# Performance work log

Measured on AMD Instinct MI355X. Metric: run time of the kernel, lower is better.

## Reference

```python
import jax, jax.numpy as jnp
import numpy as np

B, S, D = 1, 2048, 4096          # batch, seqlen, model dim
H, KVH, HD = 32, 8, 128          # query heads, kv heads, head dim
W = 1024                         # sliding window
ROPE_THETA = 10000.0


def _rope(t, cos, sin):
    # t: [b, s, h, hd]; complex pairing matches torch.view_as_complex on reshape(..., hd//2, 2)
    a = t[..., 0::2]
    b = t[..., 1::2]
    out_r = a * cos - b * sin
    out_i = a * sin + b * cos
    return jnp.stack([out_r, out_i], axis=-1).reshape(t.shape)


def setup_inputs() -> dict:
    key = jax.random.key(0)
    ks = jax.random.split(key, 5)
    x = jax.random.normal(ks[0], (1, B, S, D), dtype=jnp.float32)
    wq = jax.random.normal(ks[1], (H * HD, D), dtype=jnp.float32) * 0.02
    wk = jax.random.normal(ks[2], (KVH * HD, D), dtype=jnp.float32) * 0.02
    wv = jax.random.normal(ks[3], (KVH * HD, D), dtype=jnp.float32) * 0.02
    wo = jax.random.normal(ks[4], (D, H * HD), dtype=jnp.float32) * 0.02
    # rotary frequencies: freqs_cis[s, hd/2] = exp(i * s * theta^{-2k/hd})
    inv_freq = 1.0 / (ROPE_THETA ** (jnp.arange(0, HD, 2, dtype=jnp.float32) / HD))
    angles = jnp.arange(S, dtype=jnp.float32)[:, None] * inv_freq[None, :]  # [S, HD/2]
    freqs_cos = jnp.cos(angles)
    freqs_sin = jnp.sin(angles)
    # sliding-window causal mask (additive)
    i = jnp.arange(S)
    allowed = (i[:, None] >= i[None, :]) & (i[:, None] - i[None, :] < W)
    mask = jnp.where(allowed, 0.0, -1e9).astype(jnp.float32)
    positions = jnp.arange(S, dtype=jnp.int64)
    return {"x": x, "wq": wq, "wk": wk, "wv": wv, "wo": wo,
            "freqs_cos": freqs_cos, "freqs_sin": freqs_sin,
            "mask": mask, "positions": positions}


def reference(x, wq, wk, wv, wo, freqs_cos, freqs_sin, mask, positions):
    xs = x[0]                                   # [B, S, D]
    xq = (xs @ wq.T).reshape(B, S, H, HD)
    xk = (xs @ wk.T).reshape(B, S, KVH, HD)
    xv = (xs @ wv.T).reshape(B, S, KVH, HD)
    cos = freqs_cos[None, :, None, :]           # [1, S, 1, HD/2]
    sin = freqs_sin[None, :, None, :]
    xq = _rope(xq, cos, sin)
    xk = _rope(xk, cos, sin)
    # GQA: repeat_interleave kv heads to match query heads (prefill path)
    rep = H // KVH
    k = jnp.repeat(xk, rep, axis=2)             # [B, S, H, HD]
    v = jnp.repeat(xv, rep, axis=2)
    scale = HD ** -0.5
    scores = jnp.einsum('bqhd,bkhd->bhqk', xq, k) * scale + mask[None, None]
    probs = jax.nn.softmax(scores, axis=-1)
    out = jnp.einsum('bhqk,bkhd->bqhd', probs, v).reshape(B, S, H * HD)
    return (out @ wo.T)[None]                   # [1, B, S, D]
```

## Files before the change

### kernel.cpp

```cpp
#include <hip/hip_runtime.h>
#include <hip/hip_bf16.h>


typedef __attribute__((ext_vector_type(8))) short short8;
typedef __attribute__((ext_vector_type(4))) float floatx4;
typedef unsigned short u16;
typedef unsigned int u32;

__device__ __forceinline__ u16 f2bf(float f) {
  u32 u = __builtin_bit_cast(u32, f);
  u32 r = u + 0x7FFFu + ((u >> 16) & 1u);
  return (u16)(r >> 16);
}

#define GLDS16(g, l)                                                     \
  __builtin_amdgcn_global_load_lds(                                      \
      (const __attribute__((address_space(1))) u32*)(g),                 \
      (__attribute__((address_space(3))) u32*)(l), 16, 0, 0)

__global__ __launch_bounds__(256) void cast_all(
    const float* __restrict__ x, const float* __restrict__ wq,
    const float* __restrict__ wk, const float* __restrict__ wv,
    const float* __restrict__ wo, u16* __restrict__ xb, u16* __restrict__ wqb,
    u16* __restrict__ wkb, u16* __restrict__ wvb, u16* __restrict__ wob) {
  const int tid = blockIdx.x * blockDim.x + threadIdx.x;
  const int stride = gridDim.x * blockDim.x;
  auto seg = [&](const float* __restrict__ in, u16* __restrict__ out, int n4) {
    for (int i = tid; i < n4; i += stride) {
      float4 v = ((const float4*)in)[i];
      ushort4 o;
      o.x = f2bf(v.x); o.y = f2bf(v.y); o.z = f2bf(v.z); o.w = f2bf(v.w);
      ((ushort4*)out)[i] = o;
    }
  };
  seg(x, xb, 2097152);
  seg(wq, wqb, 4194304);
  seg(wk, wkb, 1048576);
  seg(wv, wvb, 1048576);
  seg(wo, wob, 4194304);
}

template <int IS_QKV>
__global__ __launch_bounds__(512, 2) void gemm_t(
    const u16* __restrict__ A, const u16* __restrict__ B, void* __restrict__ Cq,
    u16* __restrict__ Ck, u16* __restrict__ Cv, const float* __restrict__ fcos,
    const float* __restrict__ fsin) {
  constexpr int BM = IS_QKV ? 256 : 128;
  constexpr int BN = IS_QKV ? 192 : 256;
  constexpr int MFR = BM / 32;
  constexpr int AH = MFR / 2;
  constexpr int NFR = BN / 64;
  constexpr int WC = BN / 4;
  constexpr int ABYTES = BM * 64;
  constexpr int BUFSZ = ABYTES + BN * 64;
  __shared__ u16 lds[3 * BUFSZ / 2];
  const int K = 4096;

  int bm, bx;
  if constexpr (IS_QKV) {
    bm = blockIdx.x & 7;
    bx = blockIdx.x >> 3;
  } else {
    const int xcd = blockIdx.x & 7;
    const int j = blockIdx.x >> 3;
    bm = xcd * 2 + (j & 1);
    bx = j >> 1;
  }
  const int m0 = bm * BM, n0 = bx * BN;

  const int t = threadIdx.x, l = t & 63, w = t >> 6;
  const int li = l & 15, g = l >> 4;
  const int wm = w >> 2, wn = w & 3;

  const int rr = t >> 2;
  const int ssw = (t & 3) ^ ((rr >> 1) & 3);
  const u16* gA = A + (size_t)(m0 + rr) * K + ssw * 8;
  const u16* gB = B + (size_t)(n0 + rr) * K + ssw * 8;
  const int dA = t * 16;

  auto stageA = [&](int p, int kt) {
    char* base = (char*)lds + p * BUFSZ;
    GLDS16(gA + kt, base + dA);
    if constexpr (IS_QKV)
      GLDS16(gA + (size_t)128 * K + kt, base + 8192 + dA);
  };
  auto stageB = [&](int p, int kt) {
    char* base = (char*)lds + p * BUFSZ + ABYTES;
    GLDS16(gB + kt, base + dA);
    if constexpr (IS_QKV) {
      if (t < 256)
        GLDS16(gB + (size_t)128 * K + kt, base + 8192 + dA);
    } else {
      GLDS16(gB + (size_t)128 * K + kt, base + 8192 + dA);
    }
  };
  auto waitL = [&]() {
    if constexpr (IS_QKV) {
      if (t < 256) asm volatile("s_waitcnt vmcnt(4)" ::: "memory");
      else         asm volatile("s_waitcnt vmcnt(3)" ::: "memory");
    } else {
      asm volatile("s_waitcnt vmcnt(3)" ::: "memory");
    }
  };

  int offA[MFR], offB[NFR];
#pragma unroll
  for (int mf = 0; mf < MFR; mf++) {
    int r = wm * (BM / 2) + mf * 16 + li;
    offA[mf] = r * 64 + ((g ^ ((r >> 1) & 3)) << 4);
  }
#pragma unroll
  for (int nf = 0; nf < NFR; nf++) {
    int r = wn * WC + nf * 16 + li;
    offB[nf] = ABYTES + r * 64 + ((g ^ ((r >> 1) & 3)) << 4);
  }

  floatx4 acc[MFR][NFR] = {};
  const int NT = K / 32;

  stageA(0, 0); stageB(0, 0);
  stageA(1, 32); stageB(1, 32);
  waitL();
  __builtin_amdgcn_s_barrier();

  int p = 0;
  for (int tt = 0; tt < NT; ++tt) {
    int p2 = p + 2; if (p2 >= 3) p2 -= 3;
    const char* ab = (const char*)lds + p * BUFSZ;
    const int kt2 = (tt + 2) * 32;
    const bool pre = (tt + 2 < NT);
    short8 afr[AH], bfr[NFR];
#pragma unroll
    for (int nf = 0; nf < NFR; nf++) bfr[nf] = *(const short8*)(ab + offB[nf]);
#pragma unroll
    for (int mf = 0; mf < AH; mf++) afr[mf] = *(const short8*)(ab + offA[mf]);
    if (pre) stageA(p2, kt2);
    __builtin_amdgcn_sched_barrier(0);
    __builtin_amdgcn_s_barrier();
    asm volatile("s_waitcnt lgkmcnt(0)" ::: "memory");
    __builtin_amdgcn_sched_barrier(0);
    __builtin_amdgcn_s_setprio(1);
#pragma unroll
    for (int mf = 0; mf < AH; mf++)
#pragma unroll
      for (int nf = 0; nf < NFR; nf++)
        acc[mf][nf] = __builtin_amdgcn_mfma_f32_16x16x32_bf16(afr[mf], bfr[nf], acc[mf][nf], 0, 0, 0);
    __builtin_amdgcn_s_setprio(0);
    __builtin_amdgcn_sched_barrier(0);
    __builtin_amdgcn_s_barrier();
#pragma unroll
    for (int mf = 0; mf < AH; mf++) afr[mf] = *(const short8*)(ab + offA[AH + mf]);
    if (pre) stageB(p2, kt2);
    __builtin_amdgcn_sched_barrier(0);
    __builtin_amdgcn_s_barrier();
    asm volatile("s_waitcnt lgkmcnt(0)" ::: "memory");
    __builtin_amdgcn_sched_barrier(0);
    __builtin_amdgcn_s_setprio(1);
#pragma unroll
    for (int mf = 0; mf < AH; mf++)
#pragma unroll
      for (int nf = 0; nf < NFR; nf++)
        acc[AH + mf][nf] = __builtin_amdgcn_mfma_f32_16x16x32_bf16(afr[mf], bfr[nf], acc[AH + mf][nf], 0, 0, 0);
    __builtin_amdgcn_s_setprio(0);
    if (pre) {
      waitL();
    } else if (tt + 1 < NT) {
      asm volatile("s_waitcnt vmcnt(0)" ::: "memory");
    }
    __builtin_amdgcn_sched_barrier(0);
    __builtin_amdgcn_s_barrier();
    p = p + 1; if (p >= 3) p -= 3;
  }

  const float scale = 0.08838834764831845f;
#pragma unroll
  for (int mf = 0; mf < MFR; mf++) {
#pragma unroll
    for (int nf = 0; nf < NFR; nf++) {
      const int row0 = m0 + wm * (BM / 2) + mf * 16 + 4 * g;
      const int c = n0 + wn * WC + nf * 16 + li;
      if constexpr (!IS_QKV) {
        float* Cf = (float*)Cq;
#pragma unroll
        for (int r = 0; r < 4; r++) Cf[(size_t)(row0 + r) * 4096 + c] = acc[mf][nf][r];
      } else {
        if (c < 5120) {
          const int hd = c & 127;
          const int pp = hd >> 1;
          const bool even = (hd & 1) == 0;
#pragma unroll
          for (int r = 0; r < 4; r++) {
            const int row = row0 + r;
            float cv = fcos[row * 64 + pp];
            float sv = fsin[row * 64 + pp];
            float v = acc[mf][nf][r];
            float pv = __shfl_xor(v, 1);
            float o = even ? (v * cv - pv * sv) : (pv * sv + v * cv);
            if (c < 4096) {
              ((u16*)Cq)[(size_t)row * 4096 + c] = f2bf(o * scale);
            } else {
              Ck[(size_t)row * 1024 + (c - 4096)] = f2bf(o);
            }
          }
        } else {
          u32 lo = (u32)f2bf(acc[mf][nf][0]) | ((u32)f2bf(acc[mf][nf][1]) << 16);
          u32 hi = (u32)f2bf(acc[mf][nf][2]) | ((u32)f2bf(acc[mf][nf][3]) << 16);
          uint2 val; val.x = lo; val.y = hi;
          *(uint2*)(&Cv[(size_t)(c - 5120) * 2048 + row0]) = val;
        }
      }
    }
  }
}

__global__ __launch_bounds__(256) void attn_kernel(const u16* __restrict__ Q,
                                                   const u16* __restrict__ K,
                                                   const u16* __restrict__ Vt,
                                                   u16* __restrict__ O) {
  __shared__ u16 Ks[2][64 * 128];
  __shared__ u16 Vs[2][128 * 64];
  __shared__ u16 Ps[4][16 * 72];

  const int t = threadIdx.x, l = t & 63, w = t >> 6;
  const int li = l & 15, g = l >> 4;
  const int q0 = blockIdx.x * 64;
  const int h = blockIdx.y;
  const int kvh = h >> 2;
  const int qw = q0 + w * 16;

  short8 qf[4];
  {
    const u16* qp = Q + (size_t)(qw + li) * 4096 + h * 128 + g * 8;
#pragma unroll
    for (int kk = 0; kk < 4; kk++) qf[kk] = *(const short8*)(qp + kk * 32);
  }

  const u16* gK[4];
  const u16* gV[4];
  int ldsOff[4];
#pragma unroll
  for (int i = 0; i < 4; i++) {
    int rK = 16 * w + 4 * i + (l >> 4);
    int sK = (l & 15) ^ (rK & 7);
    gK[i] = K + (size_t)rK * 1024 + kvh * 128 + sK * 8;
    int rV = 32 * w + 8 * i + (l >> 3);
    int sV = (l & 7) ^ (rV & 7);
    gV[i] = Vt + (size_t)(kvh * 128 + rV) * 2048 + sV * 8;
    ldsOff[i] = (4 * w + i) * 1024;
  }

  int offK[4][4];
#pragma unroll
  for (int n = 0; n < 4; n++) {
    int r = 16 * n + li;
#pragma unroll
    for (int kk = 0; kk < 4; kk++)
      offK[n][kk] = r * 256 + (((kk * 4 + g) ^ (r & 7)) << 4);
  }
  int offV[2][8];
#pragma unroll
  for (int kb = 0; kb < 2; kb++)
#pragma unroll
    for (int dt = 0; dt < 8; dt++) {
      int d = dt * 16 + li;
      offV[kb][dt] = d * 128 + (((kb * 4 + g) ^ (d & 7)) << 4);
    }

  float mrow[4] = {-1e30f, -1e30f, -1e30f, -1e30f};
  float lsum[4] = {0.f, 0.f, 0.f, 0.f};
  floatx4 accO[8] = {};

  int klo = q0 - 1023;
  if (klo < 0) klo = 0;
  klo &= ~63;
  const int nt = (q0 + 64 - klo) >> 6;

  auto stage = [&](int buf, int k0) {
    char* ksb = (char*)&Ks[buf][0];
    char* vsb = (char*)&Vs[buf][0];
#pragma unroll
    for (int i = 0; i < 4; i++) GLDS16(gK[i] + (size_t)k0 * 1024, ksb + ldsOff[i]);
#pragma unroll
    for (int i = 0; i < 4; i++) GLDS16(gV[i] + k0, vsb + ldsOff[i]);
  };

  stage(0, klo);
  asm volatile("s_waitcnt vmcnt(0)" ::: "memory");
  __builtin_amdgcn_s_barrier();

  for (int it = 0; it < nt; it++) {
    const int k0 = klo + (it << 6);
    if (it + 1 < nt) stage((it + 1) & 1, k0 + 64);

    if (k0 <= qw + 15 && k0 + 63 >= qw - 1023) {
      const char* kb = (const char*)&Ks[it & 1][0];
      const char* vb = (const char*)&Vs[it & 1][0];
      floatx4 s[4] = {};
      __builtin_amdgcn_s_setprio(1);
#pragma unroll
      for (int kk = 0; kk < 4; kk++)
#pragma unroll
        for (int n = 0; n < 4; n++) {
          short8 kf = *(const short8*)(kb + offK[n][kk]);
          s[n] = __builtin_amdgcn_mfma_f32_16x16x32_bf16(qf[kk], kf, s[n], 0, 0, 0);
        }
      __builtin_amdgcn_s_setprio(0);
      const bool full = (k0 + 63 <= qw) && (k0 >= qw + 15 - 1023);
      if (!full) {
#pragma unroll
        for (int n = 0; n < 4; n++) {
          const int kc = k0 + n * 16 + li;
#pragma unroll
          for (int r = 0; r < 4; r++) {
            const int qr = qw + 4 * g + r;
            if (kc > qr || qr - kc > 1023) s[n][r] = -__builtin_inff();
          }
        }
      }
      float rm[4];
#pragma unroll
      for (int r = 0; r < 4; r++)
        rm[r] = fmaxf(fmaxf(s[0][r], s[1][r]), fmaxf(s[2][r], s[3][r]));
#pragma unroll
      for (int msk = 1; msk <= 8; msk <<= 1)
#pragma unroll
        for (int r = 0; r < 4; r++) rm[r] = fmaxf(rm[r], __shfl_xor(rm[r], msk));
      float al[4];
#pragma unroll
      for (int r = 0; r < 4; r++) {
        float mn = fmaxf(mrow[r], rm[r]);
        al[r] = __expf(mrow[r] - mn);
        mrow[r] = mn;
        lsum[r] *= al[r];
      }
#pragma unroll
      for (int dt = 0; dt < 8; dt++)
#pragma unroll
        for (int r = 0; r < 4; r++) accO[dt][r] *= al[r];
      float rs[4] = {0.f, 0.f, 0.f, 0.f};
      u16* pw = &Ps[w][0];
#pragma unroll
      for (int n = 0; n < 4; n++)
#pragma unroll
        for (int r = 0; r < 4; r++) {
          float p = __expf(s[n][r] - mrow[r]);
          rs[r] += p;
          pw[(4 * g + r) * 72 + n * 16 + li] = f2bf(p);
        }
#pragma unroll
      for (int msk = 1; msk <= 8; msk <<= 1)
#pragma unroll
        for (int r = 0; r < 4; r++) rs[r] += __shfl_xor(rs[r], msk);
#pragma unroll
      for (int r = 0; r < 4; r++) lsum[r] += rs[r];
      short8 pa[2];
#pragma unroll
      for (int kbi = 0; kbi < 2; kbi++)
        pa[kbi] = *(const short8*)((const char*)&Ps[w][0] + li * 144 + kbi * 64 + g * 16);
      __builtin_amdgcn_s_setprio(1);
#pragma unroll
      for (int kbi = 0; kbi < 2; kbi++)
#pragma unroll
        for (int dt = 0; dt < 8; dt++) {
          short8 vf = *(const short8*)(vb + offV[kbi][dt]);
          accO[dt] = __builtin_amdgcn_mfma_f32_16x16x32_bf16(pa[kbi], vf, accO[dt], 0, 0, 0);
        }
      __builtin_amdgcn_s_setprio(0);
    }
    asm volatile("s_waitcnt vmcnt(0)" ::: "memory");
    __builtin_amdgcn_s_barrier();
  }

  float inv[4];
#pragma unroll
  for (int r = 0; r < 4; r++) inv[r] = 1.0f / lsum[r];
#pragma unroll
  for (int dt = 0; dt < 8; dt++)
#pragma unroll
    for (int r = 0; r < 4; r++)
      O[(size_t)(qw + 4 * g + r) * 4096 + h * 128 + dt * 16 + li] =
          f2bf(accO[dt][r] * inv[r]);
}

extern "C" void kernel_launch(void* const* d_in, const int* in_sizes, int n_in,
                              void* d_out, int out_size, void* d_ws, size_t ws_size,
                              hipStream_t stream) {
  const float* x    = (const float*)d_in[0];
  const float* wq   = (const float*)d_in[1];
  const float* wk   = (const float*)d_in[2];
  const float* wv   = (const float*)d_in[3];
  const float* wo   = (const float*)d_in[4];
  const float* fcos = (const float*)d_in[5];
  const float* fsin = (const float*)d_in[6];

  u16* ws  = (u16*)d_ws;
  u16* xb  = ws;
  u16* wqb = xb + 8388608;
  u16* wkb = wqb + 16777216;
  u16* wvb = wkb + 4194304;
  u16* wob = wvb + 4194304;
  u16* Qb  = wob + 16777216;
  u16* Kb  = Qb + 8388608;
  u16* Vtb = Kb + 2097152;
  u16* AOb = Vtb + 2097152;

  cast_all<<<2048, 256, 0, stream>>>(x, wq, wk, wv, wo, xb, wqb, wkb, wvb, wob);
  gemm_t<1><<<256, 512, 0, stream>>>(xb, wqb, Qb, Kb, Vtb, fcos, fsin);
  attn_kernel<<<dim3(32, 32), 256, 0, stream>>>(Qb, Kb, Vtb, AOb);
  gemm_t<0><<<256, 512, 0, stream>>>(AOb, wob, d_out, nullptr, nullptr, nullptr, nullptr);
}
```

Measured before the change: 338.3 us.

## Double K-tile to 64 with split A/B buffering and wider LDS swizzle

Reworks the bf16 GEMM main loop so each iteration covers a K tile of 64 instead of 32. A is now double-buffered and B triple-buffered, using an 8-slot XOR swizzle over 128-byte rows. Global-to-LDS staging of the next A tile and the B tile two steps ahead is spread across four MFMA phases. The aim is fewer barriers and waitcnts per unit of K and better overlap of loads with MFMA work. The cost is a larger LDS footprint, which may limit how many blocks fit per CU, most likely for the output-projection GEMM.

```diff
diff --git a/kernel.cpp b/kernel.cpp
--- a/kernel.cpp
+++ b/kernel.cpp
@@ -17,6 +17,8 @@
   __builtin_amdgcn_global_load_lds(                                      \
       (const __attribute__((address_space(1))) u32*)(g),                 \
       (__attribute__((address_space(3))) u32*)(l), 16, 0, 0)
+
+#define SB() __builtin_amdgcn_sched_barrier(0)
 
 __global__ __launch_bounds__(256) void cast_all(
     const float* __restrict__ x, const float* __restrict__ wq,
@@ -48,12 +50,13 @@
   constexpr int BM = IS_QKV ? 256 : 128;
   constexpr int BN = IS_QKV ? 192 : 256;
   constexpr int MFR = BM / 32;
-  constexpr int AH = MFR / 2;
   constexpr int NFR = BN / 64;
   constexpr int WC = BN / 4;
-  constexpr int ABYTES = BM * 64;
-  constexpr int BUFSZ = ABYTES + BN * 64;
-  __shared__ u16 lds[3 * BUFSZ / 2];
+  constexpr int ASZ = BM * 128;
+  constexpr int BSZ = BN * 128;
+  constexpr int NCA = ASZ / 8192;
+  constexpr int NCB = BSZ / 8192;
+  __shared__ u16 lds[(2 * ASZ + 3 * BSZ) / 2];
   const int K = 4096;
 
   int bm, bx;
@@ -72,104 +75,177 @@
   const int li = l & 15, g = l >> 4;
   const int wm = w >> 2, wn = w & 3;
 
-  const int rr = t >> 2;
-  const int ssw = (t & 3) ^ ((rr >> 1) & 3);
-  const u16* gA = A + (size_t)(m0 + rr) * K + ssw * 8;
-  const u16* gB = B + (size_t)(n0 + rr) * K + ssw * 8;
-  const int dA = t * 16;
-
-  auto stageA = [&](int p, int kt) {
-    char* base = (char*)lds + p * BUFSZ;
-    GLDS16(gA + kt, base + dA);
-    if constexpr (IS_QKV)
-      GLDS16(gA + (size_t)128 * K + kt, base + 8192 + dA);
+  const int srow = t >> 3;
+  const int sslot = (t & 7) ^ (srow & 7);
+  const u16* gA = A + (size_t)(m0 + srow) * K + sslot * 8;
+  const u16* gB = B + (size_t)(n0 + srow) * K + sslot * 8;
+  const int dst = t * 16;
+
+  char* A0p = (char*)lds;
+  char* A1p = A0p + ASZ;
+  char* B0p = A0p + 2 * ASZ;
+  char* B1p = B0p + BSZ;
+  char* B2p = B1p + BSZ;
+
+  auto stA = [&](char* base, int kt, int c) {
+    GLDS16(gA + (size_t)c * 64 * K + kt, base + c * 8192 + dst);
   };
-  auto stageB = [&](int p, int kt) {
-    char* base = (char*)lds + p * BUFSZ + ABYTES;
-    GLDS16(gB + kt, base + dA);
+  auto stB = [&](char* base, int kt, int c) {
+    GLDS16(gB + (size_t)c * 64 * K + kt, base + c * 8192 + dst);
+  };
+
+  int offA[2][MFR], offB[2][NFR];
+#pragma unroll
+  for (int kh = 0; kh < 2; kh++) {
+#pragma unroll
+    for (int mf = 0; mf < MFR; mf++) {
+      int r = wm * (BM / 2) + mf * 16 + li;
+      offA[kh][mf] = r * 128 + ((((kh << 2) | g) ^ (r & 7)) << 4);
+    }
+#pragma unroll
+    for (int nf = 0; nf < NFR; nf++) {
+      int r = wn * WC + nf * 16 + li;
+      offB[kh][nf] = r * 128 + ((((kh << 2) | g) ^ (r & 7)) << 4);
+    }
+  }
+
+  floatx4 acc[MFR][NFR] = {};
+  const int NT = K / 64;
+
+#pragma unroll
+  for (int c = 0; c < NCB; c++) stB(B0p, 0, c);
+#pragma unroll
+  for (int c = 0; c < NCA; c++) stA(A0p, 0, c);
+#pragma unroll
+  for (int c = 0; c < NCB; c++) stB(B1p, 64, c);
+  if constexpr (IS_QKV) asm volatile("s_waitcnt vmcnt(3)" ::: "memory");
+  else                  asm volatile("s_waitcnt vmcnt(4)" ::: "memory");
+  __builtin_amdgcn_s_barrier();
+
+  for (int tt = 0; tt < NT; ++tt) {
+    const char* Ac = A0p;
+    const char* Bc = B0p;
+    const int kt1 = (tt + 1) * 64, kt2 = (tt + 2) * 64;
+    const bool s1 = (tt + 1 < NT), s2 = (tt + 2 < NT);
+
     if constexpr (IS_QKV) {
-      if (t < 256)
-        GLDS16(gB + (size_t)128 * K + kt, base + 8192 + dA);
+      short8 afr[4], bfr[NFR];
+#pragma unroll
+      for (int nf = 0; nf < NFR; nf++) bfr[nf] = *(const short8*)(Bc + offB[0][nf]);
+#pragma unroll
+      for (int mf = 0; mf < 4; mf++) afr[mf] = *(const short8*)(Ac + offA[0][mf]);
+      if (s1) { stA(A1p, kt1, 0); stA(A1p, kt1, 1); }
+      SB(); __builtin_amdgcn_s_barrier();
+      asm volatile("s_waitcnt lgkmcnt(0)" ::: "memory");
+      SB(); __builtin_amdgcn_s_setprio(1);
+#pragma unroll
+      for (int mf = 0; mf < 4; mf++)
+#pragma unroll
+        for (int nf = 0; nf < NFR; nf++)
+          acc[mf][nf] = __builtin_amdgcn_mfma_f32_16x16x32_bf16(afr[mf], bfr[nf], acc[mf][nf], 0, 0, 0);
+      __builtin_amdgcn_s_setprio(0); SB(); __builtin_amdgcn_s_barrier();
+#pragma unroll
+      for (int mf = 0; mf < 4; mf++) afr[mf] = *(const short8*)(Ac + offA[0][4 + mf]);
+      if (s1) { stA(A1p, kt1, 2); stA(A1p, kt1, 3); }
+      SB(); __builtin_amdgcn_s_barrier();
+      asm volatile("s_waitcnt lgkmcnt(0)" ::: "memory");
+      SB(); __builtin_amdgcn_s_setprio(1);
+#pragma unroll
+      for (int mf = 0; mf < 4; mf++)
+#pragma unroll
+        for (int nf = 0; nf < NFR; nf++)
+          acc[4 + mf][nf] = __builtin_amdgcn_mfma_f32_16x16x32_bf16(afr[mf], bfr[nf], acc[4 + mf][nf], 0, 0, 0);
+      __builtin_amdgcn_s_setprio(0); SB(); __builtin_amdgcn_s_barrier();
+#pragma unroll
+      for (int nf = 0; nf < NFR; nf++) bfr[nf] = *(const short8*)(Bc + offB[1][nf]);
+#pragma unroll
+      for (int mf = 0; mf < 4; mf++) afr[mf] = *(const short8*)(Ac + offA[1][mf]);
+      if (s2) { stB(B2p, kt2, 0); stB(B2p, kt2, 1); }
+      SB(); __builtin_amdgcn_s_barrier();
+      asm volatile("s_waitcnt lgkmcnt(0)" ::: "memory");
+      SB(); __builtin_amdgcn_s_setprio(1);
+#pragma unroll
+      for (int mf = 0; mf < 4; mf++)
+#pragma unroll
+        for (int nf = 0; nf < NFR; nf++)
+          acc[mf][nf] = __builtin_amdgcn_mfma_f32_16x16x32_bf16(afr[mf], bfr[nf], acc[mf][nf], 0, 0, 0);
+      __builtin_amdgcn_s_setprio(0); SB(); __builtin_amdgcn_s_barrier();
+#pragma unroll
+      for (int mf = 0; mf < 4; mf++) afr[mf] = *(const short8*)(Ac + offA[1][4 + mf]);
+      if (s2) stB(B2p, kt2, 2);
+      SB(); __builtin_amdgcn_s_barrier();
+      asm volatile("s_waitcnt lgkmcnt(0)" ::: "memory");
+      SB(); __builtin_amdgcn_s_setprio(1);
+#pragma unroll
+      for (int mf = 0; mf < 4; mf++)
+#pragma unroll
+        for (int nf = 0; nf < NFR; nf++)
+          acc[4 + mf][nf] = __builtin_amdgcn_mfma_f32_16x16x32_bf16(afr[mf], bfr[nf], acc[4 + mf][nf], 0, 0, 0);
+      __builtin_amdgcn_s_setprio(0);
+      if (s2) asm volatile("s_waitcnt vmcnt(3)" ::: "memory");
+      else    asm volatile("s_waitcnt vmcnt(0)" ::: "memory");
+      SB(); __builtin_amdgcn_s_barrier();
     } else {
-      GLDS16(gB + (size_t)128 * K + kt, base + 8192 + dA);
-    }
-  };
-  auto waitL = [&]() {
-    if constexpr (IS_QKV) {
-      if (t < 256) asm volatile("s_waitcnt vmcnt(4)" ::: "memory");
-      else         asm volatile("s_waitcnt vmcnt(3)" ::: "memory");
-    } else {
-      asm volatile("s_waitcnt vmcnt(3)" ::: "memory");
-    }
-  };
-
-  int offA[MFR], offB[NFR];
-#pragma unroll
-  for (int mf = 0; mf < MFR; mf++) {
-    int r = wm * (BM / 2) + mf * 16 + li;
-    offA[mf] = r * 64 + ((g ^ ((r >> 1) & 3)) << 4);
-  }
-#pragma unroll
-  for (int nf = 0; nf < NFR; nf++) {
-    int r = wn * WC + nf * 16 + li;
-    offB[nf] = ABYTES + r * 64 + ((g ^ ((r >> 1) & 3)) << 4);
-  }
-
-  floatx4 acc[MFR][NFR] = {};
-  const int NT = K / 32;
-
-  stageA(0, 0); stageB(0, 0);
-  stageA(1, 32); stageB(1, 32);
-  waitL();
-  __builtin_amdgcn_s_barrier();
-
-  int p = 0;
-  for (int tt = 0; tt < NT; ++tt) {
-    int p2 = p + 2; if (p2 >= 3) p2 -= 3;
-    const char* ab = (const char*)lds + p * BUFSZ;
-    const int kt2 = (tt + 2) * 32;
-    const bool pre = (tt + 2 < NT);
-    short8 afr[AH], bfr[NFR];
-#pragma unroll
-    for (int nf = 0; nf < NFR; nf++) bfr[nf] = *(const short8*)(ab + offB[nf]);
-#pragma unroll
-    for (int mf = 0; mf < AH; mf++) afr[mf] = *(const short8*)(ab + offA[mf]);
-    if (pre) stageA(p2, kt2);
-    __builtin_amdgcn_sched_barrier(0);
-    __builtin_amdgcn_s_barrier();
-    asm volatile("s_waitcnt lgkmcnt(0)" ::: "memory");
-    __builtin_amdgcn_sched_barrier(0);
-    __builtin_amdgcn_s_setprio(1);
-#pragma unroll
-    for (int mf = 0; mf < AH; mf++)
-#pragma unroll
-      for (int nf = 0; nf < NFR; nf++)
-        acc[mf][nf] = __builtin_amdgcn_mfma_f32_16x16x32_bf16(afr[mf], bfr[nf], acc[mf][nf], 0, 0, 0);
-    __builtin_amdgcn_s_setprio(0);
-    __builtin_amdgcn_sched_barrier(0);
-    __builtin_amdgcn_s_barrier();
-#pragma unroll
-    for (int mf = 0; mf < AH; mf++) afr[mf] = *(const short8*)(ab + offA[AH + mf]);
-    if (pre) stageB(p2, kt2);
-    __builtin_amdgcn_sched_barrier(0);
-    __builtin_amdgcn_s_barrier();
-    asm volatile("s_waitcnt lgkmcnt(0)" ::: "memory");
-    __builtin_amdgcn_sched_barrier(0);
-    __builtin_amdgcn_s_setprio(1);
-#pragma unroll
-    for (int mf = 0; mf < AH; mf++)
-#pragma unroll
-      for (int nf = 0; nf < NFR; nf++)
-        acc[AH + mf][nf] = __builtin_amdgcn_mfma_f32_16x16x32_bf16(afr[mf], bfr[nf], acc[AH + mf][nf], 0, 0, 0);
-    __builtin_amdgcn_s_setprio(0);
-    if (pre) {
-      waitL();
-    } else if (tt + 1 < NT) {
-      asm volatile("s_waitcnt vmcnt(0)" ::: "memory");
-    }
-    __builtin_amdgcn_sched_barrier(0);
-    __builtin_amdgcn_s_barrier();
-    p = p + 1; if (p >= 3) p -= 3;
+      short8 afr[4], bfr[2];
+#pragma unroll
+      for (int mf = 0; mf < 4; mf++) afr[mf] = *(const short8*)(Ac + offA[0][mf]);
+#pragma unroll
+      for (int nf = 0; nf < 2; nf++) bfr[nf] = *(const short8*)(Bc + offB[0][nf]);
+      if (s1) { stA(A1p, kt1, 0); stA(A1p, kt1, 1); }
+      SB(); __builtin_amdgcn_s_barrier();
+      asm volatile("s_waitcnt lgkmcnt(0)" ::: "memory");
+      SB(); __builtin_amdgcn_s_setprio(1);
+#pragma unroll
+      for (int mf = 0; mf < 4; mf++)
+#pragma unroll
+        for (int nf = 0; nf < 2; nf++)
+          acc[mf][nf] = __builtin_amdgcn_mfma_f32_16x16x32_bf16(afr[mf], bfr[nf], acc[mf][nf], 0, 0, 0);
+      __builtin_amdgcn_s_setprio(0); SB(); __builtin_amdgcn_s_barrier();
+#pragma unroll
+      for (int nf = 0; nf < 2; nf++) bfr[nf] = *(const short8*)(Bc + offB[0][2 + nf]);
+      if (s2) { stB(B2p, kt2, 0); stB(B2p, kt2, 1); }
+      SB(); __builtin_amdgcn_s_barrier();
+      asm volatile("s_waitcnt lgkmcnt(0)" ::: "memory");
+      SB(); __builtin_amdgcn_s_setprio(1);
+#pragma unroll
+      for (int mf = 0; mf < 4; mf++)
+#pragma unroll
+        for (int nf = 0; nf < 2; nf++)
+          acc[mf][2 + nf] = __builtin_amdgcn_mfma_f32_16x16x32_bf16(afr[mf], bfr[nf], acc[mf][2 + nf], 0, 0, 0);
+      __builtin_amdgcn_s_setprio(0); SB(); __builtin_amdgcn_s_barrier();
+#pragma unroll
+      for (int mf = 0; mf < 4; mf++) afr[mf] = *(const short8*)(Ac + offA[1][mf]);
+#pragma unroll
+      for (int nf = 0; nf < 2; nf++) bfr[nf] = *(const short8*)(Bc + offB[1][nf]);
+      if (s2) stB(B2p, kt2, 2);
+      SB(); __builtin_amdgcn_s_barrier();
+      asm volatile("s_waitcnt lgkmcnt(0)" ::: "memory");
+      SB(); __builtin_amdgcn_s_setprio(1);
+#pragma unroll
+      for (int mf = 0; mf < 4; mf++)
+#pragma unroll
+        for (int nf = 0; nf < 2; nf++)
+          acc[mf][nf] = __builtin_amdgcn_mfma_f32_16x16x32_bf16(afr[mf], bfr[nf], acc[mf][nf], 0, 0, 0);
+      __builtin_amdgcn_s_setprio(0); SB(); __builtin_amdgcn_s_barrier();
+#pragma unroll
+      for (int nf = 0; nf < 2; nf++) bfr[nf] = *(const short8*)(Bc + offB[1][2 + nf]);
+      if (s2) stB(B2p, kt2, 3);
+      SB(); __builtin_amdgcn_s_barrier();
+      asm volatile("s_waitcnt lgkmcnt(0)" ::: "memory");
+      SB(); __builtin_amdgcn_s_setprio(1);
+#pragma unroll
+      for (int mf = 0; mf < 4; mf++)
+#pragma unroll
+        for (int nf = 0; nf < 2; nf++)
+          acc[mf][2 + nf] = __builtin_amdgcn_mfma_f32_16x16x32_bf16(afr[mf], bfr[nf], acc[mf][2 + nf], 0, 0, 0);
+      __builtin_amdgcn_s_setprio(0);
+      if (s2) asm volatile("s_waitcnt vmcnt(4)" ::: "memory");
+      else    asm volatile("s_waitcnt vmcnt(0)" ::: "memory");
+      SB(); __builtin_amdgcn_s_barrier();
+    }
+
+    char* tmpA = A0p; A0p = A1p; A1p = tmpA;
+    char* tmpB = B0p; B0p = B1p; B1p = B2p; B2p = tmpB;
   }
 
   const float scale = 0.08838834764831845f;
```

New measurement: 321.0 us. -5.1%, faster.
